# Kernel optimization log

Hardware: AMD Instinct MI355X
Metric: run time of the kernel (lower is better)

Reference implementation:

```python
import jax, jax.numpy as jnp
import numpy as np

N = 50000   # nodes
E = 800000  # edges
F = 128     # input features
H = 4       # heads
C = 32      # hidden per head
ED = 16     # edge_dim
NEG_ATT = 0.2   # GATConv leaky relu slope for attention
NEG_OUT = 0.01  # nn.LeakyReLU default slope in GATLayer


def setup_inputs() -> dict:
    key = jax.random.key(0)
    ks = jax.random.split(key, 9)
    s = 0.05
    return {
        "node_features": jax.random.normal(ks[0], (N, F), jnp.float32),
        "edge_index": jax.random.randint(ks[1], (2, E), 0, N, dtype=jnp.int32),
        "edge_attr": jax.random.normal(ks[2], (E, ED), jnp.float32),
        "W": jax.random.normal(ks[3], (F, H * C), jnp.float32) * s,
        "W_edge": jax.random.normal(ks[4], (ED, H * C), jnp.float32) * s,
        "att_src": jax.random.normal(ks[5], (H, C), jnp.float32) * s,
        "att_dst": jax.random.normal(ks[6], (H, C), jnp.float32) * s,
        "att_edge": jax.random.normal(ks[7], (H, C), jnp.float32) * s,
        "bias": jax.random.normal(ks[8], (H * C,), jnp.float32) * s,
    }


def reference(node_features, edge_index, edge_attr, W, W_edge, att_src, att_dst, att_edge, bias):
    # Project nodes: [N, H, C]  (PyG GATConv with int in_channels shares lin for src/dst)
    x = (node_features @ W).reshape(N, H, C)
    a_src = jnp.einsum('nhc,hc->nh', x, att_src)  # [N, H]
    a_dst = jnp.einsum('nhc,hc->nh', x, att_dst)  # [N, H]

    src, dst = edge_index[0], edge_index[1]

    # add_self_loops with fill_value='mean': self-loop edge_attr = mean of incoming edge attrs
    cnt = jax.ops.segment_sum(jnp.ones((E,), jnp.float32), dst, num_segments=N)
    loop_attr = jax.ops.segment_sum(edge_attr, dst, num_segments=N) / jnp.clip(cnt, 1.0)[:, None]
    ar = jnp.arange(N, dtype=src.dtype)
    src_f = jnp.concatenate([src, ar])          # [E+N]
    dst_f = jnp.concatenate([dst, ar])          # [E+N]
    ea_f = jnp.concatenate([edge_attr, loop_attr], axis=0)  # [E+N, ED]

    # Edge attention contribution
    e = (ea_f @ W_edge).reshape(E + N, H, C)
    a_edge = jnp.einsum('ehc,hc->eh', e, att_edge)  # [E+N, H]

    # Raw attention logits per edge/head, LeakyReLU(0.2)
    alpha = a_src[src_f] + a_dst[dst_f] + a_edge
    alpha = jax.nn.leaky_relu(alpha, NEG_ATT)

    # Softmax over incoming edges per target node (stable; every node has self loop)
    m = jax.ops.segment_max(alpha, dst_f, num_segments=N)      # [N, H]
    ex = jnp.exp(alpha - m[dst_f])                              # [E+N, H]
    denom = jax.ops.segment_sum(ex, dst_f, num_segments=N)     # [N, H]
    attn = ex / denom[dst_f]                                    # [E+N, H]

    # Scatter-aggregate weighted source features
    msgs = x[src_f] * attn[:, :, None]                          # [E+N, H, C]
    out = jax.ops.segment_sum(msgs, dst_f, num_segments=N)      # [N, H, C]
    out = out.reshape(N, H * C) + bias

    # GATLayer wrapper: LeakyReLU(0.01) then Dropout(p=0) (identity)
    return jax.nn.leaky_relu(out, NEG_OUT)
```

## Files before the change

kernel.cpp:

```cpp
#include <hip/hip_runtime.h>

typedef unsigned short u16;
typedef unsigned int u32;
typedef unsigned long long u64;
typedef short bf16x8 __attribute__((ext_vector_type(8)));
typedef float f32x4  __attribute__((ext_vector_type(4)));

#define NN 50000
#define EE 800000
#define CAP 48
#define GBLK ((NN+31)/32)

__device__ __forceinline__ float lrelu(float x, float s){ return x>=0.f ? x : s*x; }
__device__ __forceinline__ u16 f2bf(float f){ u32 x=__float_as_uint(f); u32 r=(x+0x7fffu+((x>>16)&1u))>>16; return (u16)r; }
__device__ __forceinline__ float bf2f_lo(u32 u){ union{u32 i; float f;} v; v.i=u<<16; return v.f; }
__device__ __forceinline__ float bf2f_hi(u32 u){ union{u32 i; float f;} v; v.i=u&0xffff0000u; return v.f; }

__global__ __launch_bounds__(256) void k_wcvt(const float* __restrict__ W,
                                              u16* __restrict__ WF){
    int t = threadIdx.x;
    int l = t & 63;
    int cell = blockIdx.x*4 + (t >> 6);
    int kb = cell >> 3, ct = cell & 7;
    int kbase = kb*32 + ((l >> 4) << 3);
    int c = ct*16 + (l & 15);
    u16 fr[8];
    #pragma unroll
    for (int j = 0; j < 8; j++)
        fr[j] = f2bf(W[(size_t)(kbase + j)*128 + c]);
    uint4 pk;
    pk.x = fr[0] | ((u32)fr[1] << 16);
    pk.y = fr[2] | ((u32)fr[3] << 16);
    pk.z = fr[4] | ((u32)fr[5] << 16);
    pk.w = fr[6] | ((u32)fr[7] << 16);
    *(uint4*)&WF[(size_t)(cell*64 + l) << 3] = pk;
}

__global__ __launch_bounds__(256) void k_pre(const float* __restrict__ A,
                                             const u16*   __restrict__ WF,
                                             const float* __restrict__ att_src,
                                             const float* __restrict__ att_dst,
                                             const int*   __restrict__ ei,
                                             const float* __restrict__ ea,
                                             const float* __restrict__ W_edge,
                                             const float* __restrict__ att_edge,
                                             u32* __restrict__ xb,
                                             float* __restrict__ asd,
                                             int* __restrict__ cnt,
                                             u64* __restrict__ csr,
                                             u32* __restrict__ pae){
    __shared__ float wea[64];
    int t = threadIdx.x;
    int bid = blockIdx.x;
    int g = bid / 3, r = bid - g*3;

    if (r == 2){
        int r0 = g * 32;
        int w = t >> 6, l = t & 63;
        int rh = w >> 1, ctb = (w & 1) * 4, h0 = (w & 1) * 2;
        int col = l & 15, kg = l >> 4;
        int arow = r0 + rh*16 + col;

        bf16x8 af[4];
        #pragma unroll
        for (int kb = 0; kb < 4; kb++){
            float4 v0 = make_float4(0.f,0.f,0.f,0.f);
            float4 v1 = make_float4(0.f,0.f,0.f,0.f);
            if (arow < NN){
                const float* ap = A + (size_t)arow*128 + kb*32 + kg*8;
                v0 = *(const float4*)ap;
                v1 = *(const float4*)(ap + 4);
            }
            bf16x8 a;
            a[0]=f2bf(v0.x); a[1]=f2bf(v0.y); a[2]=f2bf(v0.z); a[3]=f2bf(v0.w);
            a[4]=f2bf(v1.x); a[5]=f2bf(v1.y); a[6]=f2bf(v1.z); a[7]=f2bf(v1.w);
            af[kb] = a;
        }

        f32x4 acc[4] = {};
        #pragma unroll
        for (int kb = 0; kb < 4; kb++){
            #pragma unroll
            for (int c4 = 0; c4 < 4; c4++){
                bf16x8 bfr = *(const bf16x8*)&WF[(size_t)((kb*8 + ctb + c4)*64 + l) << 3];
                acc[c4] = __builtin_amdgcn_mfma_f32_16x16x32_bf16(af[kb], bfr, acc[c4], 0, 0, 0);
            }
        }

        float as_c[4], ad_c[4];
        #pragma unroll
        for (int c4 = 0; c4 < 4; c4++){
            as_c[c4] = att_src[(ctb+c4)*16 + col];
            ad_c[c4] = att_dst[(ctb+c4)*16 + col];
        }
        #pragma unroll
        for (int reg = 0; reg < 4; reg++){
            int gr = r0 + rh*16 + kg*4 + reg;
            float x0 = acc[0][reg], x1 = acc[1][reg], x2 = acc[2][reg], x3 = acc[3][reg];
            float s0 = x0*as_c[0] + x1*as_c[1];
            float s1 = x2*as_c[2] + x3*as_c[3];
            float d0 = x0*ad_c[0] + x1*ad_c[1];
            float d1 = x2*ad_c[2] + x3*ad_c[3];
            #pragma unroll
            for (int m = 1; m < 16; m <<= 1){
                s0 += __shfl_xor(s0, m, 64);
                s1 += __shfl_xor(s1, m, 64);
                d0 += __shfl_xor(d0, m, 64);
                d1 += __shfl_xor(d1, m, 64);
            }
            if (gr < NN){
                if (col == 0){
                    *(float2*)&asd[gr*8 + h0]     = make_float2(s0, s1);
                    *(float2*)&asd[gr*8 + 4 + h0] = make_float2(d0, d1);
                }
                u16* xo = (u16*)xb + (size_t)gr*128 + col;
                xo[(ctb+0)*16] = f2bf(x0);
                xo[(ctb+1)*16] = f2bf(x1);
                xo[(ctb+2)*16] = f2bf(x2);
                xo[(ctb+3)*16] = f2bf(x3);
            }
        }
    } else {
        if (t < 64){
            int hh = t >> 4, d = t & 15;
            float s = 0.f;
            #pragma unroll
            for (int c = 0; c < 32; c++)
                s += W_edge[d*128 + hh*32 + c] * att_edge[hh*32 + c];
            wea[t] = s;
        }
        __syncthreads();

        int e = (g*2 + r)*256 + t;
        if (e >= EE) return;
        int src = ei[e];
        int dst = ei[EE + e];
        const float4* p = (const float4*)(ea + (size_t)e*16);
        float4 q0 = p[0], q1 = p[1], q2 = p[2], q3 = p[3];
        float f[16] = {q0.x,q0.y,q0.z,q0.w, q1.x,q1.y,q1.z,q1.w,
                       q2.x,q2.y,q2.z,q2.w, q3.x,q3.y,q3.z,q3.w};
        float sh[4];
        #pragma unroll
        for (int h = 0; h < 4; h++){
            float s = 0.f;
            #pragma unroll
            for (int d = 0; d < 16; d++) s += f[d]*wea[h*16+d];
            sh[h] = s;
        }
        u32 p01 = (u32)f2bf(sh[0]) | ((u32)f2bf(sh[1]) << 16);
        u32 p23 = (u32)f2bf(sh[2]) | ((u32)f2bf(sh[3]) << 16);
        *(uint2*)&pae[(size_t)e*2] = make_uint2(p01, p23);
        int slot = atomicAdd(&cnt[dst], 1);
        if (slot < CAP)
            __builtin_nontemporal_store(((u64)(u32)src << 32) | (u32)e,
                                        &csr[(size_t)dst*CAP + slot]);
    }
}

__global__ __launch_bounds__(256) void k_agg(const u32* __restrict__ xb,
                                             const float* __restrict__ asd,
                                             const int* __restrict__ cnt,
                                             const u64* __restrict__ csr,
                                             const u32* __restrict__ pae,
                                             const float* __restrict__ bias,
                                             float* __restrict__ out){
    int lane = threadIdx.x & 63, wvi = threadIdx.x >> 6;
    int n = blockIdx.x*4 + wvi;
    if (n >= NN) return;
    int h = lane >> 4, j16 = lane & 15, e4 = lane >> 2, hl = lane & 3;
    int dgc = cnt[n];
    int dg = min(dgc, CAP);
    int start = n*CAP;
    float ad_n = asd[n*8 + 4 + hl];

    float denom = 0.f, acc0 = 0.f, acc1 = 0.f, sum_ae = 0.f;
    for (int base = 0; base < dg; base += 16){
        u64 pr = csr[start + base + j16];
        bool vj = base + j16 < dg;
        int eid = vj ? (int)(pr & 0xffffffffu) : 0;
        int sj  = vj ? (int)(pr >> 32)         : 0;
        int eid_p = __shfl(eid, e4, 64);
        int src_p = __shfl(sj, e4, 64);
        u32 aw = pae[(u32)eid_p*2 + (hl >> 1)];
        float ae = (hl & 1) ? bf2f_hi(aw) : bf2f_lo(aw);
        bool v4 = base + e4 < dg;
        float as_v = asd[src_p*8 + hl];
        float alpha = lrelu(as_v + ad_n + ae, 0.2f);
        float wv = v4 ? __expf(alpha) : 0.f;
        sum_ae += v4 ? ae : 0.f;
        #pragma unroll
        for (int j = 0; j < 16; j++){
            float wj = __shfl(wv, j*4 + h, 64);
            int s   = __shfl(sj, j, 64);
            u32 xp = xb[((u32)s << 6) | lane];
            denom += wj;
            acc0 += wj * bf2f_lo(xp);
            acc1 += wj * bf2f_hi(xp);
        }
    }
    #pragma unroll
    for (int s = 4; s < 64; s <<= 1) sum_ae += __shfl_xor(sum_ae, s, 64);
    float sae = __shfl(sum_ae, h, 64);

    float ael = sae / fmaxf((float)dgc, 1.f);
    float al_loop = lrelu(asd[n*8 + h] + asd[n*8 + 4 + h] + ael, 0.2f);
    float wl = __expf(al_loop);
    u32 xn = xb[((u32)n << 6) | lane];
    denom += wl;
    acc0 += wl * bf2f_lo(xn);
    acc1 += wl * bf2f_hi(xn);

    float inv = 1.f / denom;
    float2 bv = *(const float2*)&bias[2*lane];
    float o0 = lrelu(acc0*inv + bv.x, 0.01f);
    float o1 = lrelu(acc1*inv + bv.y, 0.01f);
    *(float2*)&out[(size_t)n*128 + 2*lane] = make_float2(o0, o1);
}

extern "C" void kernel_launch(void* const* d_in, const int* in_sizes, int n_in,
                              void* d_out, int out_size, void* d_ws, size_t ws_size,
                              hipStream_t stream){
    const float* node_features = (const float*)d_in[0];
    const int*   edge_index    = (const int*)d_in[1];
    const float* edge_attr     = (const float*)d_in[2];
    const float* W             = (const float*)d_in[3];
    const float* W_edge        = (const float*)d_in[4];
    const float* att_src       = (const float*)d_in[5];
    const float* att_dst       = (const float*)d_in[6];
    const float* att_edge      = (const float*)d_in[7];
    const float* bias          = (const float*)d_in[8];
    float* out = (float*)d_out;

    char* p = (char*)d_ws;
    auto alloc = [&](size_t b)->char*{ char* r = p; p += ((b + 255)/256)*256; return r; };
    u32*   xb  = (u32*)  alloc((size_t)NN*64*4);
    float* asd = (float*)alloc((size_t)NN*8*4);
    int*   cnt = (int*)  alloc((size_t)NN*4);
    u64*   csr = (u64*)  alloc((size_t)NN*CAP*8);
    u32*   pae = (u32*)  alloc((size_t)EE*8);
    u16*   WF  = (u16*)  alloc((size_t)32*64*8*2);

    (void)hipMemsetAsync(cnt, 0, (size_t)NN*4, stream);

    k_wcvt<<<dim3(8), dim3(256), 0, stream>>>(W, WF);
    k_pre<<<dim3(3*GBLK), dim3(256), 0, stream>>>(
        node_features, WF, att_src, att_dst,
        edge_index, edge_attr, W_edge, att_edge,
        xb, asd, cnt, csr, pae);
    k_agg<<<dim3((NN+3)/4), dim3(256), 0, stream>>>(
        xb, asd, cnt, csr, pae, bias, out);
}
```

Baseline: 217.3 us.

## Hoist edge-attention weight fold out of k_pre and process two edges per thread

```diff
diff --git a/kernel.cpp b/kernel.cpp
--- a/kernel.cpp
+++ b/kernel.cpp
@@ -17,8 +17,19 @@
 __device__ __forceinline__ float bf2f_hi(u32 u){ union{u32 i; float f;} v; v.i=u&0xffff0000u; return v.f; }
 
 __global__ __launch_bounds__(256) void k_wcvt(const float* __restrict__ W,
-                                              u16* __restrict__ WF){
+                                              const float* __restrict__ W_edge,
+                                              const float* __restrict__ att_edge,
+                                              u16* __restrict__ WF,
+                                              float* __restrict__ weaG){
     int t = threadIdx.x;
+    if (blockIdx.x == 0 && t < 64){
+        int hh = t >> 4, d = t & 15;
+        float s = 0.f;
+        #pragma unroll
+        for (int c = 0; c < 32; c++)
+            s += W_edge[d*128 + hh*32 + c] * att_edge[hh*32 + c];
+        weaG[t] = s;
+    }
     int l = t & 63;
     int cell = blockIdx.x*4 + (t >> 6);
     int kb = cell >> 3, ct = cell & 7;
@@ -42,8 +53,7 @@
                                              const float* __restrict__ att_dst,
                                              const int*   __restrict__ ei,
                                              const float* __restrict__ ea,
-                                             const float* __restrict__ W_edge,
-                                             const float* __restrict__ att_edge,
+                                             const float* __restrict__ weaG,
                                              u32* __restrict__ xb,
                                              float* __restrict__ asd,
                                              int* __restrict__ cnt,
@@ -52,9 +62,10 @@
     __shared__ float wea[64];
     int t = threadIdx.x;
     int bid = blockIdx.x;
-    int g = bid / 3, r = bid - g*3;
-
-    if (r == 2){
+    int g = bid >> 1;
+    int r = (bid ^ (bid >> 3)) & 1;
+
+    if (r == 0){
         int r0 = g * 32;
         int w = t >> 6, l = t & 63;
         int rh = w >> 1, ctb = (w & 1) * 4, h0 = (w & 1) * 2;
@@ -121,39 +132,55 @@
             }
         }
     } else {
-        if (t < 64){
-            int hh = t >> 4, d = t & 15;
-            float s = 0.f;
+        if (t < 64) wea[t] = weaG[t];
+        __syncthreads();
+
+        int e0 = (g << 9) + t;
+        int e1 = e0 + 256;
+        bool v1 = e1 < EE;
+        int src0 = ei[e0],            dst0 = ei[EE + e0];
+        int src1 = v1 ? ei[e1] : 0;
+        int dst1 = v1 ? ei[EE + e1] : 0;
+        const float4* p0 = (const float4*)(ea + (size_t)e0*16);
+        const float4* p1 = (const float4*)(ea + (size_t)e1*16);
+        float4 a0 = p0[0], a1 = p0[1], a2 = p0[2], a3 = p0[3];
+        float4 b0 = make_float4(0,0,0,0), b1 = b0, b2 = b0, b3 = b0;
+        if (v1){ b0 = p1[0]; b1 = p1[1]; b2 = p1[2]; b3 = p1[3]; }
+        int slot0 = atomicAdd(&cnt[dst0], 1);
+        int slot1 = v1 ? atomicAdd(&cnt[dst1], 1) : CAP;
+
+        float f0[16] = {a0.x,a0.y,a0.z,a0.w, a1.x,a1.y,a1.z,a1.w,
+                        a2.x,a2.y,a2.z,a2.w, a3.x,a3.y,a3.z,a3.w};
+        float f1[16] = {b0.x,b0.y,b0.z,b0.w, b1.x,b1.y,b1.z,b1.w,
+                        b2.x,b2.y,b2.z,b2.w, b3.x,b3.y,b3.z,b3.w};
+        float sh0[4], sh1[4];
+        #pragma unroll
+        for (int h = 0; h < 4; h++){
+            float s0 = 0.f, s1 = 0.f;
             #pragma unroll
-            for (int c = 0; c < 32; c++)
-                s += W_edge[d*128 + hh*32 + c] * att_edge[hh*32 + c];
-            wea[t] = s;
-        }
-        __syncthreads();
-
-        int e = (g*2 + r)*256 + t;
-        if (e >= EE) return;
-        int src = ei[e];
-        int dst = ei[EE + e];
-        const float4* p = (const float4*)(ea + (size_t)e*16);
-        float4 q0 = p[0], q1 = p[1], q2 = p[2], q3 = p[3];
-        float f[16] = {q0.x,q0.y,q0.z,q0.w, q1.x,q1.y,q1.z,q1.w,
-                       q2.x,q2.y,q2.z,q2.w, q3.x,q3.y,q3.z,q3.w};
-        float sh[4];
-        #pragma unroll
-        for (int h = 0; h < 4; h++){
-            float s = 0.f;
-            #pragma unroll
-            for (int d = 0; d < 16; d++) s += f[d]*wea[h*16+d];
-            sh[h] = s;
-        }
-        u32 p01 = (u32)f2bf(sh[0]) | ((u32)f2bf(sh[1]) << 16);
-        u32 p23 = (u32)f2bf(sh[2]) | ((u32)f2bf(sh[3]) << 16);
-        *(uint2*)&pae[(size_t)e*2] = make_uint2(p01, p23);
-        int slot = atomicAdd(&cnt[dst], 1);
-        if (slot < CAP)
-            __builtin_nontemporal_store(((u64)(u32)src << 32) | (u32)e,
-                                        &csr[(size_t)dst*CAP + slot]);
+            for (int d = 0; d < 16; d++){
+                float wv = wea[h*16+d];
+                s0 += f0[d]*wv;
+                s1 += f1[d]*wv;
+            }
+            sh0[h] = s0; sh1[h] = s1;
+        }
+        {
+            u32 p01 = (u32)f2bf(sh0[0]) | ((u32)f2bf(sh0[1]) << 16);
+            u32 p23 = (u32)f2bf(sh0[2]) | ((u32)f2bf(sh0[3]) << 16);
+            *(uint2*)&pae[(size_t)e0*2] = make_uint2(p01, p23);
+        }
+        if (v1){
+            u32 p01 = (u32)f2bf(sh1[0]) | ((u32)f2bf(sh1[1]) << 16);
+            u32 p23 = (u32)f2bf(sh1[2]) | ((u32)f2bf(sh1[3]) << 16);
+            *(uint2*)&pae[(size_t)e1*2] = make_uint2(p01, p23);
+        }
+        if (slot0 < CAP)
+            __builtin_nontemporal_store(((u64)(u32)src0 << 32) | (u32)e0,
+                                        &csr[(size_t)dst0*CAP + slot0]);
+        if (v1 && slot1 < CAP)
+            __builtin_nontemporal_store(((u64)(u32)src1 << 32) | (u32)e1,
+                                        &csr[(size_t)dst1*CAP + slot1]);
     }
 }
 
@@ -233,19 +260,20 @@
 
     char* p = (char*)d_ws;
     auto alloc = [&](size_t b)->char*{ char* r = p; p += ((b + 255)/256)*256; return r; };
-    u32*   xb  = (u32*)  alloc((size_t)NN*64*4);
-    float* asd = (float*)alloc((size_t)NN*8*4);
-    int*   cnt = (int*)  alloc((size_t)NN*4);
-    u64*   csr = (u64*)  alloc((size_t)NN*CAP*8);
-    u32*   pae = (u32*)  alloc((size_t)EE*8);
-    u16*   WF  = (u16*)  alloc((size_t)32*64*8*2);
+    u32*   xb   = (u32*)  alloc((size_t)NN*64*4);
+    float* asd  = (float*)alloc((size_t)NN*8*4);
+    int*   cnt  = (int*)  alloc((size_t)NN*4);
+    u64*   csr  = (u64*)  alloc((size_t)NN*CAP*8);
+    u32*   pae  = (u32*)  alloc((size_t)EE*8);
+    u16*   WF   = (u16*)  alloc((size_t)32*64*8*2);
+    float* weaG = (float*)alloc(64*4);
 
     (void)hipMemsetAsync(cnt, 0, (size_t)NN*4, stream);
 
-    k_wcvt<<<dim3(8), dim3(256), 0, stream>>>(W, WF);
-    k_pre<<<dim3(3*GBLK), dim3(256), 0, stream>>>(
+    k_wcvt<<<dim3(8), dim3(256), 0, stream>>>(W, W_edge, att_edge, WF, weaG);
+    k_pre<<<dim3(2*GBLK), dim3(256), 0, stream>>>(
         node_features, WF, att_src, att_dst,
-        edge_index, edge_attr, W_edge, att_edge,
+        edge_index, edge_attr, weaG,
         xb, asd, cnt, csr, pae);
     k_agg<<<dim3((NN+3)/4), dim3(256), 0, stream>>>(
         xb, asd, cnt, csr, pae, bias, out);
```

Measured after the change: 218.9 us. About the same (+0.8%).
